# Kernel tuning notes

Measured on AMD Instinct MI355X. Metric: run time of the kernel, lower is better.

## Reference

```python
import jax, jax.numpy as jnp
import numpy as np

OUT_F, IN_F, GROUP_SIZE = 4096, 4096, 64
N_GROUPS = OUT_F * IN_F // GROUP_SIZE  # 262144
B, S = 8, 2048


def setup_inputs() -> dict:
    key = jax.random.key(0)
    k1, k2, k3, k4, k5 = jax.random.split(key, 5)
    x = jax.random.normal(k1, (B, S, IN_F), dtype=jnp.float32)
    # packed 8-bit weights: '8bit_u8' packing is a plain uint8 store (values 0..255)
    W_q = jax.random.randint(k2, (GROUP_SIZE, N_GROUPS), 0, 256, dtype=jnp.int32)
    # per-group dequant params: scale = 1/quant_scale (small), zero = quant zero-point
    scale = jax.random.uniform(k3, (1, N_GROUPS), dtype=jnp.float32) * 0.01 + 1e-4
    zero = jax.random.uniform(k4, (1, N_GROUPS), dtype=jnp.float32) * 255.0
    bias = jax.random.normal(k5, (OUT_F,), dtype=jnp.float32)
    return {"x": x, "W_q": W_q, "scale": scale, "zero": zero, "bias": bias}


def reference(x, W_q, scale, zero, bias):
    # Quantizer.dequantize: unpack (identity for 8bit_u8), then ((W_q - zero) * scale).reshape(shape)
    W_r = ((W_q.astype(x.dtype) - zero) * scale).reshape(OUT_F, IN_F)  # [out, in]
    # forward_pytorch: F.linear(x, W_r, bias)
    return jnp.einsum("bsi,oi->bso", x, W_r) + bias
```

## Files before the change

### kernel.cpp

```cpp
#include <hip/hip_runtime.h>
#include <cstdio>
#include <cstdint>
#include <cstddef>

#define AS_GLOBAL __attribute__((address_space(1)))
#define AS_LDS    __attribute__((address_space(3)))

typedef __bf16 bf16x8 __attribute__((ext_vector_type(8)));
typedef float  f32x4  __attribute__((ext_vector_type(4)));

constexpr int OUT_F = 4096;
constexpr int IN_F  = 4096;
constexpr int MROWS = 8 * 2048;

__global__ void dequant_w(const int* __restrict__ Wq, const float* __restrict__ scale,
                          const float* __restrict__ zero, __bf16* __restrict__ Wb) {
    int t   = blockIdx.x * blockDim.x + threadIdx.x;
    int idx = t * 4;
    int o   = idx >> 12;
    int i   = idx & 4095;
    int n   = ((o & 63) << 12) | i;
    size_t flat = ((size_t)(o >> 6) << 18) + (size_t)n;
    int4   q = *(const int4*)(Wq + flat);
    float4 z = *(const float4*)(zero + n);
    float4 s = *(const float4*)(scale + n);
    __bf16 r[4];
    r[0] = (__bf16)(((float)q.x - z.x) * s.x);
    r[1] = (__bf16)(((float)q.y - z.y) * s.y);
    r[2] = (__bf16)(((float)q.z - z.z) * s.z);
    r[3] = (__bf16)(((float)q.w - z.w) * s.w);
    *(uint2*)(Wb + idx) = *(const uint2*)r;
}

__global__ void convert_x(const float* __restrict__ x, __bf16* __restrict__ xb) {
    size_t t   = (size_t)blockIdx.x * blockDim.x + threadIdx.x;
    size_t idx = t * 8;
    float4 a = *(const float4*)(x + idx);
    float4 b = *(const float4*)(x + idx + 4);
    __bf16 r[8];
    r[0] = (__bf16)a.x; r[1] = (__bf16)a.y; r[2] = (__bf16)a.z; r[3] = (__bf16)a.w;
    r[4] = (__bf16)b.x; r[5] = (__bf16)b.y; r[6] = (__bf16)b.z; r[7] = (__bf16)b.w;
    *(uint4*)(xb + idx) = *(const uint4*)r;
}

__device__ __forceinline__ void load16_to_lds(const void* g, void* lds) {
    __builtin_amdgcn_global_load_lds((AS_GLOBAL void*)g, (AS_LDS void*)lds, 16, 0, 0);
}

__global__ __launch_bounds__(256) void gemm_bt_bias(
    const __bf16* __restrict__ A,
    const __bf16* __restrict__ B,
    const float*  __restrict__ bias,
    float*        __restrict__ C)
{
    constexpr int K = IN_F, N = OUT_F;
    constexpr int BKt = 32;
    __shared__ __align__(16) __bf16 sA[128 * BKt];
    __shared__ __align__(16) __bf16 sB[128 * BKt];

    const int tid  = threadIdx.x;
    const int lane = tid & 63;
    const int w    = tid >> 6;
    const int wr   = w >> 1;
    const int wc   = w & 1;
    const int m0   = blockIdx.y * 128;
    const int n0   = blockIdx.x * 128;

    f32x4 acc[4][4] = {};

    const int r0 = tid >> 2;
    const int cc = (tid & 3) * 8;
    const __bf16* gA0 = A + (size_t)(m0 + r0) * K + cc;
    const __bf16* gA1 = gA0 + (size_t)64 * K;
    const __bf16* gB0 = B + (size_t)(n0 + r0) * K + cc;
    const __bf16* gB1 = gB0 + (size_t)64 * K;
    char* sAb = (char*)sA + w * 1024;
    char* sBb = (char*)sB + w * 1024;

    const int fr = lane & 15;
    const int fk = (lane >> 4) * 8;

    for (int k0 = 0; k0 < K; k0 += BKt) {
        __syncthreads();
        load16_to_lds(gA0 + k0, sAb);
        load16_to_lds(gA1 + k0, sAb + 4096);
        load16_to_lds(gB0 + k0, sBb);
        load16_to_lds(gB1 + k0, sBb + 4096);
        __syncthreads();

        bf16x8 aF[4], bF[4];
#pragma unroll
        for (int mi = 0; mi < 4; ++mi)
            aF[mi] = *(const bf16x8*)(sA + (wr * 64 + mi * 16 + fr) * BKt + fk);
#pragma unroll
        for (int ni = 0; ni < 4; ++ni)
            bF[ni] = *(const bf16x8*)(sB + (wc * 64 + ni * 16 + fr) * BKt + fk);
#pragma unroll
        for (int mi = 0; mi < 4; ++mi)
#pragma unroll
            for (int ni = 0; ni < 4; ++ni)
                acc[mi][ni] = __builtin_amdgcn_mfma_f32_16x16x32_bf16(
                    aF[mi], bF[ni], acc[mi][ni], 0, 0, 0);
    }

    const int rb = (lane >> 4) * 4;
    const int cl = lane & 15;
#pragma unroll
    for (int ni = 0; ni < 4; ++ni) {
        const int   c  = n0 + wc * 64 + ni * 16 + cl;
        const float bv = bias[c];
#pragma unroll
        for (int mi = 0; mi < 4; ++mi) {
            const size_t base = (size_t)(m0 + wr * 64 + mi * 16 + rb) * N + c;
#pragma unroll
            for (int rg = 0; rg < 4; ++rg)
                C[base + (size_t)rg * N] = acc[mi][ni][rg] + bv;
        }
    }
}

extern "C" void kernel_launch(void* const* d_in, const int* in_sizes, int n_in,
                              void* d_out, int out_size, void* d_ws, size_t ws_size,
                              hipStream_t stream) {
    const float* x     = (const float*)d_in[0];
    const int*   Wq    = (const int*)d_in[1];
    const float* scale = (const float*)d_in[2];
    const float* zero  = (const float*)d_in[3];
    const float* bias  = (const float*)d_in[4];
    float* out = (float*)d_out;

    const size_t wbytes = (size_t)OUT_F * IN_F * 2;
    const size_t xbytes = (size_t)MROWS * IN_F * 2;
    if (ws_size < wbytes + xbytes) {
        fprintf(stderr, "kernel_launch: ws_size=%zu < needed %zu — aborting\n",
                ws_size, wbytes + xbytes);
        return;
    }
    __bf16* Wb = (__bf16*)d_ws;
    __bf16* xb = (__bf16*)((char*)d_ws + wbytes);

    dequant_w<<<(OUT_F * IN_F / 4) / 256, 256, 0, stream>>>(Wq, scale, zero, Wb);
    convert_x<<<((size_t)MROWS * IN_F / 8) / 256, 256, 0, stream>>>(x, xb);

    dim3 grid(OUT_F / 128, MROWS / 128);
    gemm_bt_bias<<<grid, 256, 0, stream>>>(xb, Wb, bias, out);
}
```

Baseline: 1.090 ms.

## Rewrite GEMM with 256x256 tiles, 4-stage LDS pipeline, swizzle and XCD remap

Replaces the 128x128 single-buffered GEMM with a 512-thread kernel that computes 256x256 output tiles. It keeps four LDS buffers filled by async global-to-LDS loads, using vmcnt waits and raw barriers so loads overlap MFMA work. Other changes: an XOR swizzle on the LDS layout to avoid bank conflicts, a block-index remap that groups tiles per XCD for L2 reuse, and s_setprio around the MFMA bursts. The cost is 128KB of LDS per block, which limits occupancy to one block per CU, and more accumulator registers per thread.

Result: faster. 937.3 us (-14.0%).

```diff
diff --git a/kernel.cpp b/kernel.cpp
--- a/kernel.cpp
+++ b/kernel.cpp
@@ -47,71 +47,107 @@
     __builtin_amdgcn_global_load_lds((AS_GLOBAL void*)g, (AS_LDS void*)lds, 16, 0, 0);
 }
 
-__global__ __launch_bounds__(256) void gemm_bt_bias(
+__global__ __launch_bounds__(512, 2) void gemm256(
     const __bf16* __restrict__ A,
     const __bf16* __restrict__ B,
     const float*  __restrict__ bias,
     float*        __restrict__ C)
 {
-    constexpr int K = IN_F, N = OUT_F;
-    constexpr int BKt = 32;
-    __shared__ __align__(16) __bf16 sA[128 * BKt];
-    __shared__ __align__(16) __bf16 sB[128 * BKt];
+    constexpr int K   = IN_F, N = OUT_F;
+    constexpr int BK  = 32;
+    constexpr int NT  = K / BK;
+    constexpr int BUF = 32768;
+    __shared__ __align__(16) char smem[4 * BUF];
 
-    const int tid  = threadIdx.x;
-    const int lane = tid & 63;
-    const int w    = tid >> 6;
-    const int wr   = w >> 1;
-    const int wc   = w & 1;
-    const int m0   = blockIdx.y * 128;
-    const int n0   = blockIdx.x * 128;
+    const int tid = threadIdx.x;
+    const int l   = tid & 63;
+    const int w   = tid >> 6;
+    const int wr  = w >> 2;
+    const int wc  = w & 3;
 
-    f32x4 acc[4][4] = {};
+    const int bid = blockIdx.x;
+    const int wg  = (bid & 7) * 128 + (bid >> 3);
+    const int n0  = (wg & 15) * 256;
+    const int m0  = (wg >> 4) * 256;
 
-    const int r0 = tid >> 2;
-    const int cc = (tid & 3) * 8;
-    const __bf16* gA0 = A + (size_t)(m0 + r0) * K + cc;
-    const __bf16* gA1 = gA0 + (size_t)64 * K;
-    const __bf16* gB0 = B + (size_t)(n0 + r0) * K + cc;
-    const __bf16* gB1 = gB0 + (size_t)64 * K;
-    char* sAb = (char*)sA + w * 1024;
-    char* sBb = (char*)sB + w * 1024;
+    const int srow   = l >> 2;
+    const int schunk = (l & 3) ^ ((l >> 3) & 3);
+    const __bf16* sA0 = A + (size_t)(m0 + (w*2+0)*16 + srow) * K + schunk*8;
+    const __bf16* sA1 = A + (size_t)(m0 + (w*2+1)*16 + srow) * K + schunk*8;
+    const __bf16* sB0 = B + (size_t)(n0 + (w*2+0)*16 + srow) * K + schunk*8;
+    const __bf16* sB1 = B + (size_t)(n0 + (w*2+1)*16 + srow) * K + schunk*8;
+    const int dstA0 = (w*2+0)*1024, dstA1 = (w*2+1)*1024;
+    const int dstB0 = 16384 + dstA0, dstB1 = 16384 + dstA1;
 
-    const int fr = lane & 15;
-    const int fk = (lane >> 4) * 8;
+    const int fr = l & 15, fg = l >> 4;
+    const int in_off = fr*64 + ((fg ^ ((fr >> 1) & 3)) << 4);
 
-    for (int k0 = 0; k0 < K; k0 += BKt) {
-        __syncthreads();
-        load16_to_lds(gA0 + k0, sAb);
-        load16_to_lds(gA1 + k0, sAb + 4096);
-        load16_to_lds(gB0 + k0, sBb);
-        load16_to_lds(gB1 + k0, sBb + 4096);
-        __syncthreads();
+    f32x4 acc[8][4] = {};
 
-        bf16x8 aF[4], bF[4];
-#pragma unroll
-        for (int mi = 0; mi < 4; ++mi)
-            aF[mi] = *(const bf16x8*)(sA + (wr * 64 + mi * 16 + fr) * BKt + fk);
-#pragma unroll
-        for (int ni = 0; ni < 4; ++ni)
-            bF[ni] = *(const bf16x8*)(sB + (wc * 64 + ni * 16 + fr) * BKt + fk);
-#pragma unroll
-        for (int mi = 0; mi < 4; ++mi)
-#pragma unroll
-            for (int ni = 0; ni < 4; ++ni)
-                acc[mi][ni] = __builtin_amdgcn_mfma_f32_16x16x32_bf16(
-                    aF[mi], bF[ni], acc[mi][ni], 0, 0, 0);
+#define STAGE(t) do {                                                   \
+        char* _b = smem + ((t) & 3) * BUF;                              \
+        const int _k = (t) * BK;                                        \
+        load16_to_lds(sA0 + _k, _b + dstA0);                            \
+        load16_to_lds(sA1 + _k, _b + dstA1);                            \
+        load16_to_lds(sB0 + _k, _b + dstB0);                            \
+        load16_to_lds(sB1 + _k, _b + dstB1);                            \
+    } while (0)
+
+#define COMPUTE(t) do {                                                 \
+        const char* _a  = smem + ((t) & 3) * BUF;                       \
+        const char* _bb = _a + 16384;                                   \
+        bf16x8 aF[8], bF[4];                                            \
+        _Pragma("unroll")                                               \
+        for (int mi = 0; mi < 8; ++mi)                                  \
+            aF[mi] = *(const bf16x8*)(_a + (wr*8 + mi)*1024 + in_off);  \
+        _Pragma("unroll")                                               \
+        for (int ni = 0; ni < 4; ++ni)                                  \
+            bF[ni] = *(const bf16x8*)(_bb + (wc*4 + ni)*1024 + in_off); \
+        __builtin_amdgcn_s_setprio(1);                                  \
+        _Pragma("unroll")                                               \
+        for (int mi = 0; mi < 8; ++mi)                                  \
+            _Pragma("unroll")                                           \
+            for (int ni = 0; ni < 4; ++ni)                              \
+                acc[mi][ni] = __builtin_amdgcn_mfma_f32_16x16x32_bf16(  \
+                    aF[mi], bF[ni], acc[mi][ni], 0, 0, 0);              \
+        __builtin_amdgcn_s_setprio(0);                                  \
+    } while (0)
+
+    STAGE(0); STAGE(1); STAGE(2);
+    asm volatile("s_waitcnt vmcnt(8)" ::: "memory");
+    asm volatile("s_barrier" ::: "memory");
+
+#pragma unroll 4
+    for (int T = 0; T < NT - 4; ++T) {
+        STAGE(T + 3);
+        COMPUTE(T);
+        asm volatile("s_waitcnt vmcnt(8)" ::: "memory");
+        asm volatile("s_barrier" ::: "memory");
     }
+    STAGE(NT - 1);
+    COMPUTE(NT - 4);
+    asm volatile("s_waitcnt vmcnt(8)" ::: "memory");
+    asm volatile("s_barrier" ::: "memory");
+    COMPUTE(NT - 3);
+    asm volatile("s_waitcnt vmcnt(4)" ::: "memory");
+    asm volatile("s_barrier" ::: "memory");
+    COMPUTE(NT - 2);
+    asm volatile("s_waitcnt vmcnt(0)" ::: "memory");
+    asm volatile("s_barrier" ::: "memory");
+    COMPUTE(NT - 1);
 
-    const int rb = (lane >> 4) * 4;
-    const int cl = lane & 15;
+#undef STAGE
+#undef COMPUTE
+
+    const int rb = (l >> 4) * 4;
+    const int cl = l & 15;
 #pragma unroll
     for (int ni = 0; ni < 4; ++ni) {
         const int   c  = n0 + wc * 64 + ni * 16 + cl;
         const float bv = bias[c];
 #pragma unroll
-        for (int mi = 0; mi < 4; ++mi) {
-            const size_t base = (size_t)(m0 + wr * 64 + mi * 16 + rb) * N + c;
+        for (int mi = 0; mi < 8; ++mi) {
+            const size_t base = (size_t)(m0 + wr * 128 + mi * 16 + rb) * N + c;
 #pragma unroll
             for (int rg = 0; rg < 4; ++rg)
                 C[base + (size_t)rg * N] = acc[mi][ni][rg] + bv;
@@ -142,6 +178,6 @@
     dequant_w<<<(OUT_F * IN_F / 4) / 256, 256, 0, stream>>>(Wq, scale, zero, Wb);
     convert_x<<<((size_t)MROWS * IN_F / 8) / 256, 256, 0, stream>>>(x, xb);
 
-    dim3 grid(OUT_F / 128, MROWS / 128);
-    gemm_bt_bias<<<grid, 256, 0, stream>>>(xb, Wb, bias, out);
+    gemm256<<<dim3((MROWS / 256) * (OUT_F / 256)), dim3(512), 0, stream>>>(
+        xb, Wb, bias, out);
 }
```
